# Kernel optimization log

Hardware: AMD Instinct MI355X
Metric: run time of the kernel (lower is better)

Reference implementation:

```python
import jax, jax.numpy as jnp
import numpy as np

B, T, DIN, DM, NC = 8, 4096, 1024, 256, 157
DILS = (1, 2, 4, 8, 16)


def _conv1(w, x, b=None):
    # 1x1 conv: w [out,in], x [B,in,T] -> [B,out,T]
    y = jnp.einsum('oi,bit->bot', w, x)
    return y if b is None else y + b[None, :, None]


def _dal(x, wq, wk, wv, d):
    # Dilated 3-tap multiplicative local attention (DAL block, groups=1).
    # Taps in the zero-padded (pad=d) sequence at offsets 0, d, 2d == positions t-d, t, t+d.
    _, _, T_ = x.shape
    xp = jnp.pad(x, ((0, 0), (0, 0), (d, d)))
    q = _conv1(wq, x)                 # [B,C,T]
    kp = _conv1(wk, xp)               # [B,C,T+2d]
    vp = _conv1(wv, xp)
    k = jnp.stack([kp[:, :, 0:T_], kp[:, :, d:T_ + d], kp[:, :, 2 * d:T_ + 2 * d]], axis=-1)  # [B,C,T,3]
    v = jnp.stack([vp[:, :, 0:T_], vp[:, :, d:T_ + d], vp[:, :, 2 * d:T_ + 2 * d]], axis=-1)
    attn = jax.nn.softmax(q[..., None] * k, axis=-1)  # softmax over the 3 taps
    return jnp.sum(attn * v, axis=-1)  # [B,C,T]


def _fwd(x, mask, bottle0_w, bottle0_b,
         dal1_wq, dal1_wk, dal1_wv, bottle1_w, bottle1_b,
         dal2_wq, dal2_wk, dal2_wv, bottle2_w, bottle2_b,
         dal3_wq, dal3_wk, dal3_wv, bottle3_w, bottle3_b,
         dal4_wq, dal4_wk, dal4_wv, bottle4_w, bottle4_b,
         dal5_wq, dal5_wk, dal5_wv, bottle5_w, bottle5_b,
         bottle6_w, bottle6_b):
    m = mask[:, 0:1, :]
    out = _conv1(bottle0_w, x, bottle0_b)
    layers = [
        (dal1_wq, dal1_wk, dal1_wv, bottle1_w, bottle1_b),
        (dal2_wq, dal2_wk, dal2_wv, bottle2_w, bottle2_b),
        (dal3_wq, dal3_wk, dal3_wv, bottle3_w, bottle3_b),
        (dal4_wq, dal4_wk, dal4_wv, bottle4_w, bottle4_b),
        (dal5_wq, dal5_wk, dal5_wv, bottle5_w, bottle5_b),
    ]
    # Dropout layers are identity in eval mode.
    for (wq, wk, wv, bw, bb), d in zip(layers, DILS):
        h = jax.nn.relu(_dal(out, wq, wk, wv, d))
        h = _conv1(bw, h, bb)
        out = (out + h) * m
    return _conv1(bottle6_w, out, bottle6_b) * m  # [B,NC,T]


def setup_inputs() -> dict:
    key = jax.random.key(0)
    ks = jax.random.split(key, 32)
    s = 0.05
    inp = {}
    inp['x'] = jax.random.normal(ks[0], (B, DIN, T), jnp.float32)
    inp['mask'] = jnp.ones((B, 1, T), jnp.float32)
    inp['bottle0_w'] = jax.random.normal(ks[1], (DM, DIN), jnp.float32) * s
    inp['bottle0_b'] = jnp.zeros((DM,), jnp.float32)
    i = 2
    for l in range(1, 6):
        inp['dal%d_wq' % l] = jax.random.normal(ks[i], (DM, DM), jnp.float32) * s; i += 1
        inp['dal%d_wk' % l] = jax.random.normal(ks[i], (DM, DM), jnp.float32) * s; i += 1
        inp['dal%d_wv' % l] = jax.random.normal(ks[i], (DM, DM), jnp.float32) * s; i += 1
        inp['bottle%d_w' % l] = jax.random.normal(ks[i], (DM, DM), jnp.float32) * s; i += 1
        inp['bottle%d_b' % l] = jnp.zeros((DM,), jnp.float32)
    inp['bottle6_w'] = jax.random.normal(ks[i], (NC, DM), jnp.float32) * s
    inp['bottle6_b'] = jnp.zeros((NC,), jnp.float32)
    return inp


def reference(x, mask, bottle0_w, bottle0_b,
              dal1_wq, dal1_wk, dal1_wv, bottle1_w, bottle1_b,
              dal2_wq, dal2_wk, dal2_wv, bottle2_w, bottle2_b,
              dal3_wq, dal3_wk, dal3_wv, bottle3_w, bottle3_b,
              dal4_wq, dal4_wk, dal4_wv, bottle4_w, bottle4_b,
              dal5_wq, dal5_wk, dal5_wv, bottle5_w, bottle5_b,
              bottle6_w, bottle6_b):
    return _fwd(x, mask, bottle0_w, bottle0_b,
                dal1_wq, dal1_wk, dal1_wv, bottle1_w, bottle1_b,
                dal2_wq, dal2_wk, dal2_wv, bottle2_w, bottle2_b,
                dal3_wq, dal3_wk, dal3_wv, bottle3_w, bottle3_b,
                dal4_wq, dal4_wk, dal4_wv, bottle4_w, bottle4_b,
                dal5_wq, dal5_wk, dal5_wv, bottle5_w, bottle5_b,
                bottle6_w, bottle6_b)
```

## Files before the change

### kernel.cpp

```cpp
#include <hip/hip_runtime.h>
#include <hip/hip_bf16.h>
#include <stdint.h>

#define T_LEN 4096
#define B_SZ  8
#define D_IN  1024
#define D_M   256
#define N_C   157

typedef __attribute__((ext_vector_type(8))) short short8;
typedef __attribute__((ext_vector_type(4))) float floatx4;

static __device__ __forceinline__ unsigned short f2bf(float f) {
  unsigned u = __float_as_uint(f);
  u += 0x7FFFu + ((u >> 16) & 1u);
  return (unsigned short)(u >> 16);
}
static __device__ __forceinline__ float bf2f(unsigned short h) {
  return __uint_as_float(((unsigned)h) << 16);
}

struct WSeg { const float* src; int n; int off; };
struct WPrepArgs { WSeg seg[22]; };

__global__ void wprep_kernel(WPrepArgs a, unsigned short* __restrict__ wbuf) {
  WSeg s = a.seg[blockIdx.x];
  for (int i = (blockIdx.y << 8) + threadIdx.x; i < s.n; i += (gridDim.y << 8))
    wbuf[s.off + i] = f2bf(s.src[i]);
}

__global__ void transpose_xT(const float* __restrict__ x,
                             unsigned short* __restrict__ xT) {
  __shared__ float tile[64][65];
  const int t0 = blockIdx.x << 6;
  const int i0 = blockIdx.y << 6;
  const int b  = blockIdx.z;
  const int tid = threadIdx.x;
  {
    const int row = tid >> 2;
    const int cc  = (tid & 3) << 4;
    const float* src = x + ((size_t)b * D_IN + (i0 + row)) * T_LEN + t0 + cc;
#pragma unroll
    for (int p = 0; p < 4; ++p) {
      float4 v = *(const float4*)(src + p * 4);
      tile[row][cc + p * 4 + 0] = v.x;
      tile[row][cc + p * 4 + 1] = v.y;
      tile[row][cc + p * 4 + 2] = v.z;
      tile[row][cc + p * 4 + 3] = v.w;
    }
  }
  __syncthreads();
#pragma unroll
  for (int it = 0; it < 2; ++it) {
    const int task = tid + (it << 8);
    const int tr = task >> 3;
    const int ic = (task & 7) << 3;
    short8 o;
#pragma unroll
    for (int j = 0; j < 8; ++j) o[j] = (short)f2bf(tile[ic + j][tr]);
    *(short8*)(xT + ((size_t)b * T_LEN + (t0 + tr)) * D_IN + i0 + ic) = o;
  }
}

template<bool HAS_BIAS, bool HAS_RES, bool HAS_MASK, bool WRITE_F32,
         bool WRITE_BF16, bool OUT_CT>
__global__ __launch_bounds__(256)
void gemm_kernel(const unsigned short* __restrict__ Xact,
                 const unsigned short* __restrict__ W,
                 const float* __restrict__ bias,
                 const float* __restrict__ resid,
                 const float* __restrict__ mask,
                 float* __restrict__ outF,
                 unsigned short* __restrict__ outB,
                 int K, int Mw) {
  constexpr int LDS_LD = 72;
  __shared__ unsigned short sA[128 * LDS_LD];
  __shared__ unsigned short sB[128 * LDS_LD];

  const int t0 = blockIdx.x << 7;
  const int n0 = blockIdx.y << 7;
  const int b  = blockIdx.z;
  const int tid = threadIdx.x;
  const int wv   = tid >> 6;
  const int lane = tid & 63;
  const int wm = (wv >> 1) << 6;
  const int wn = (wv & 1) << 6;
  const int fm = lane & 15;
  const int fq = lane >> 4;

  const unsigned short* Xb = Xact + (size_t)b * T_LEN * (size_t)K;

  const floatx4 fz = {0.f, 0.f, 0.f, 0.f};
  floatx4 acc[4][4];
#pragma unroll
  for (int i = 0; i < 4; ++i)
#pragma unroll
    for (int j = 0; j < 4; ++j) acc[i][j] = fz;

  for (int kk = 0; kk < K; kk += 64) {
#pragma unroll
    for (int it = 0; it < 4; ++it) {
      int c = tid + (it << 8);
      int m = c >> 3;
      int ko = (c & 7) << 3;
      *(short8*)&sA[m * LDS_LD + ko] =
          *(const short8*)(Xb + (size_t)(t0 + m) * K + (kk + ko));
    }
#pragma unroll
    for (int it = 0; it < 4; ++it) {
      int c = tid + (it << 8);
      int n = c >> 3;
      int ko = (c & 7) << 3;
      short8 val = {0, 0, 0, 0, 0, 0, 0, 0};
      if (n0 + n < Mw)
        val = *(const short8*)(W + (size_t)(n0 + n) * K + (kk + ko));
      *(short8*)&sB[n * LDS_LD + ko] = val;
    }
    __syncthreads();
#pragma unroll
    for (int ks = 0; ks < 64; ks += 32) {
      short8 af[4], bfr[4];
#pragma unroll
      for (int i = 0; i < 4; ++i)
        af[i] = *(short8*)&sA[(wm + (i << 4) + fm) * LDS_LD + ks + (fq << 3)];
#pragma unroll
      for (int j = 0; j < 4; ++j)
        bfr[j] = *(short8*)&sB[(wn + (j << 4) + fm) * LDS_LD + ks + (fq << 3)];
#pragma unroll
      for (int i = 0; i < 4; ++i)
#pragma unroll
        for (int j = 0; j < 4; ++j)
          acc[i][j] = __builtin_amdgcn_mfma_f32_16x16x32_bf16(
              af[i], bfr[j], acc[i][j], 0, 0, 0);
    }
    __syncthreads();
  }

#pragma unroll
  for (int i = 0; i < 4; ++i) {
#pragma unroll
    for (int j = 0; j < 4; ++j) {
      const int co = n0 + wn + (j << 4) + fm;
      if (co >= Mw) continue;
      const float bi = HAS_BIAS ? bias[co] : 0.0f;
#pragma unroll
      for (int r = 0; r < 4; ++r) {
        const int t = t0 + wm + (i << 4) + (fq << 2) + r;
        float val = acc[i][j][r] + bi;
        const size_t idx = ((size_t)b * T_LEN + t) * (size_t)Mw + co;
        if (HAS_RES) val += resid[idx];
        if (HAS_MASK) val *= mask[(size_t)b * T_LEN + t];
        if (WRITE_F32) {
          if (OUT_CT)
            outF[(size_t)b * Mw * T_LEN + (size_t)co * T_LEN + t] = val;
          else
            outF[idx] = val;
        }
        if (WRITE_BF16) outB[idx] = f2bf(val);
      }
    }
  }
}

__global__ void attn_kernel(const unsigned short* __restrict__ qkv,
                            unsigned short* __restrict__ hbuf, int d) {
  const int tid = threadIdx.x;
  const int t = (blockIdx.x << 3) + (tid >> 5);
  const int b = blockIdx.y;
  const int c8 = (tid & 31) << 3;
  const unsigned short* base = qkv + ((size_t)b * T_LEN + t) * 768;
  const short8 z8 = {0, 0, 0, 0, 0, 0, 0, 0};
  short8 qv = *(const short8*)(base + c8);
  short8 kc = *(const short8*)(base + 256 + c8);
  short8 vc = *(const short8*)(base + 512 + c8);
  short8 km = z8, kp = z8, vm = z8, vp = z8;
  const long off = (long)d * 768;
  if (t >= d) {
    km = *(const short8*)(base - off + 256 + c8);
    vm = *(const short8*)(base - off + 512 + c8);
  }
  if (t + d < T_LEN) {
    kp = *(const short8*)(base + off + 256 + c8);
    vp = *(const short8*)(base + off + 512 + c8);
  }
  short8 o;
#pragma unroll
  for (int e = 0; e < 8; ++e) {
    float q  = bf2f((unsigned short)qv[e]);
    float s0 = q * bf2f((unsigned short)km[e]);
    float s1 = q * bf2f((unsigned short)kc[e]);
    float s2 = q * bf2f((unsigned short)kp[e]);
    float mx = fmaxf(s0, fmaxf(s1, s2));
    float e0 = __expf(s0 - mx), e1 = __expf(s1 - mx), e2 = __expf(s2 - mx);
    float num = e0 * bf2f((unsigned short)vm[e]) +
                e1 * bf2f((unsigned short)vc[e]) +
                e2 * bf2f((unsigned short)vp[e]);
    float r = num / (e0 + e1 + e2);
    o[e] = (short)f2bf(fmaxf(r, 0.0f));
  }
  *(short8*)(hbuf + ((size_t)b * T_LEN + t) * D_M + c8) = o;
}

extern "C" void kernel_launch(void* const* d_in, const int* in_sizes, int n_in,
                              void* d_out, int out_size, void* d_ws, size_t ws_size,
                              hipStream_t stream) {
  const float* x    = (const float*)d_in[0];
  const float* mask = (const float*)d_in[1];

  char* ws = (char*)d_ws;
  unsigned short* xT   = (unsigned short*)ws;
  unsigned short* qkv  = xT;
  float*          outF = (float*)(ws + 67108864);
  unsigned short* outB = (unsigned short*)(ws + 100663296);
  unsigned short* hbuf = (unsigned short*)(ws + 117440512);
  unsigned short* wbuf = (unsigned short*)(ws + 134217728);

  const int WB0  = 0;
  const int WQKV = 262144;
  const int WBT  = 1245184;
  const int WB6  = 1572864;

  WPrepArgs pa;
  int si = 0;
  pa.seg[si++] = { (const float*)d_in[2], 262144, WB0 };
  for (int l = 0; l < 5; ++l) {
    int bi = 4 + l * 5;
    pa.seg[si++] = { (const float*)d_in[bi + 0], 65536, WQKV + l * 196608 };
    pa.seg[si++] = { (const float*)d_in[bi + 1], 65536, WQKV + l * 196608 + 65536 };
    pa.seg[si++] = { (const float*)d_in[bi + 2], 65536, WQKV + l * 196608 + 131072 };
    pa.seg[si++] = { (const float*)d_in[bi + 3], 65536, WBT + l * 65536 };
  }
  pa.seg[si++] = { (const float*)d_in[29], 40192, WB6 };

  wprep_kernel<<<dim3(22, 64), 256, 0, stream>>>(pa, wbuf);
  transpose_xT<<<dim3(64, 16, 8), 256, 0, stream>>>(x, xT);

  gemm_kernel<true, false, false, true, true, false>
      <<<dim3(32, 2, 8), 256, 0, stream>>>(
          xT, wbuf + WB0, (const float*)d_in[3], nullptr, mask,
          outF, outB, 1024, 256);

  const int dils[5] = {1, 2, 4, 8, 16};
  for (int l = 0; l < 5; ++l) {
    int bi = 4 + l * 5;
    gemm_kernel<false, false, false, false, true, false>
        <<<dim3(32, 6, 8), 256, 0, stream>>>(
            outB, wbuf + WQKV + l * 196608, nullptr, nullptr, mask,
            nullptr, qkv, 256, 768);
    attn_kernel<<<dim3(512, 8), 256, 0, stream>>>(qkv, hbuf, dils[l]);
    gemm_kernel<true, true, true, true, true, false>
        <<<dim3(32, 2, 8), 256, 0, stream>>>(
            hbuf, wbuf + WBT + l * 65536, (const float*)d_in[bi + 4], outF, mask,
            outF, outB, 256, 256);
  }

  gemm_kernel<true, false, true, true, false, true>
      <<<dim3(32, 2, 8), 256, 0, stream>>>(
          outB, wbuf + WB6, (const float*)d_in[30], nullptr, mask,
          (float*)d_out, nullptr, 256, 157);
}
```

Baseline: 726.0 us.

## Fuse attention into bottleneck GEMM A-load and keep residual in bf16

The separate attention kernel is removed, and the dilated 3-tap softmax is now computed while staging the A operand of the following 1x1-conv GEMM. This drops the hbuf round trip and one launch per layer. The fp32 residual stream is also dropped: the residual is read from the bf16 buffer and written back in place. The grid is reordered so output-channel blocks of the same time tile run next to each other, which should help L2 reuse. As a cost, the attention math is repeated for every output-channel block (two for the 256-wide GEMM), and the residual now accumulates in bf16, which loses precision.

Measured after the change: 723.2 us. Within noise of the previous version (-0.4%).

```diff
diff --git a/kernel.cpp b/kernel.cpp
--- a/kernel.cpp
+++ b/kernel.cpp
@@ -62,23 +62,23 @@
   }
 }
 
-template<bool HAS_BIAS, bool HAS_RES, bool HAS_MASK, bool WRITE_F32,
-         bool WRITE_BF16, bool OUT_CT>
+template<bool ATTN, bool HAS_BIAS, bool HAS_RES, bool HAS_MASK,
+         bool WRITE_BF16, bool OUT_CT_F32>
 __global__ __launch_bounds__(256)
 void gemm_kernel(const unsigned short* __restrict__ Xact,
                  const unsigned short* __restrict__ W,
                  const float* __restrict__ bias,
-                 const float* __restrict__ resid,
+                 const unsigned short* __restrict__ residB,
                  const float* __restrict__ mask,
                  float* __restrict__ outF,
                  unsigned short* __restrict__ outB,
-                 int K, int Mw) {
+                 int K, int Mw, int dil) {
   constexpr int LDS_LD = 72;
   __shared__ unsigned short sA[128 * LDS_LD];
   __shared__ unsigned short sB[128 * LDS_LD];
 
-  const int t0 = blockIdx.x << 7;
-  const int n0 = blockIdx.y << 7;
+  const int n0 = blockIdx.x << 7;
+  const int t0 = blockIdx.y << 7;
   const int b  = blockIdx.z;
   const int tid = threadIdx.x;
   const int wv   = tid >> 6;
@@ -88,8 +88,10 @@
   const int fm = lane & 15;
   const int fq = lane >> 4;
 
-  const unsigned short* Xb = Xact + (size_t)b * T_LEN * (size_t)K;
-
+  const unsigned short* Xb =
+      Xact + (size_t)b * T_LEN * (size_t)(ATTN ? 768 : K);
+
+  const short8 z8 = {0, 0, 0, 0, 0, 0, 0, 0};
   const floatx4 fz = {0.f, 0.f, 0.f, 0.f};
   floatx4 acc[4][4];
 #pragma unroll
@@ -98,20 +100,60 @@
     for (int j = 0; j < 4; ++j) acc[i][j] = fz;
 
   for (int kk = 0; kk < K; kk += 64) {
-#pragma unroll
-    for (int it = 0; it < 4; ++it) {
-      int c = tid + (it << 8);
-      int m = c >> 3;
-      int ko = (c & 7) << 3;
-      *(short8*)&sA[m * LDS_LD + ko] =
-          *(const short8*)(Xb + (size_t)(t0 + m) * K + (kk + ko));
+    if constexpr (ATTN) {
+#pragma unroll
+      for (int it = 0; it < 4; ++it) {
+        int c = tid + (it << 8);
+        int m = c >> 3;
+        int ch = kk + ((c & 7) << 3);
+        int t = t0 + m;
+        const unsigned short* base = Xb + (size_t)t * 768 + ch;
+        short8 qv = *(const short8*)(base);
+        short8 kc = *(const short8*)(base + 256);
+        short8 vc = *(const short8*)(base + 512);
+        short8 km = z8, kp = z8, vm = z8, vp = z8;
+        const long off = (long)dil * 768;
+        if (t >= dil) {
+          km = *(const short8*)(base - off + 256);
+          vm = *(const short8*)(base - off + 512);
+        }
+        if (t + dil < T_LEN) {
+          kp = *(const short8*)(base + off + 256);
+          vp = *(const short8*)(base + off + 512);
+        }
+        short8 o;
+#pragma unroll
+        for (int e = 0; e < 8; ++e) {
+          float q  = bf2f((unsigned short)qv[e]);
+          float s0 = q * bf2f((unsigned short)km[e]);
+          float s1 = q * bf2f((unsigned short)kc[e]);
+          float s2 = q * bf2f((unsigned short)kp[e]);
+          float mx = fmaxf(s0, fmaxf(s1, s2));
+          float e0 = __expf(s0 - mx), e1 = __expf(s1 - mx), e2 = __expf(s2 - mx);
+          float num = e0 * bf2f((unsigned short)vm[e]) +
+                      e1 * bf2f((unsigned short)vc[e]) +
+                      e2 * bf2f((unsigned short)vp[e]);
+          float r = num / (e0 + e1 + e2);
+          o[e] = (short)f2bf(fmaxf(r, 0.0f));
+        }
+        *(short8*)&sA[m * LDS_LD + (ch - kk)] = o;
+      }
+    } else {
+#pragma unroll
+      for (int it = 0; it < 4; ++it) {
+        int c = tid + (it << 8);
+        int m = c >> 3;
+        int ko = (c & 7) << 3;
+        *(short8*)&sA[m * LDS_LD + ko] =
+            *(const short8*)(Xb + (size_t)(t0 + m) * K + (kk + ko));
+      }
     }
 #pragma unroll
     for (int it = 0; it < 4; ++it) {
       int c = tid + (it << 8);
       int n = c >> 3;
       int ko = (c & 7) << 3;
-      short8 val = {0, 0, 0, 0, 0, 0, 0, 0};
+      short8 val = z8;
       if (n0 + n < Mw)
         val = *(const short8*)(W + (size_t)(n0 + n) * K + (kk + ko));
       *(short8*)&sB[n * LDS_LD + ko] = val;
@@ -148,57 +190,14 @@
         const int t = t0 + wm + (i << 4) + (fq << 2) + r;
         float val = acc[i][j][r] + bi;
         const size_t idx = ((size_t)b * T_LEN + t) * (size_t)Mw + co;
-        if (HAS_RES) val += resid[idx];
+        if (HAS_RES) val += bf2f(residB[idx]);
         if (HAS_MASK) val *= mask[(size_t)b * T_LEN + t];
-        if (WRITE_F32) {
-          if (OUT_CT)
-            outF[(size_t)b * Mw * T_LEN + (size_t)co * T_LEN + t] = val;
-          else
-            outF[idx] = val;
-        }
+        if (OUT_CT_F32)
+          outF[(size_t)b * Mw * T_LEN + (size_t)co * T_LEN + t] = val;
         if (WRITE_BF16) outB[idx] = f2bf(val);
       }
     }
   }
-}
-
-__global__ void attn_kernel(const unsigned short* __restrict__ qkv,
-                            unsigned short* __restrict__ hbuf, int d) {
-  const int tid = threadIdx.x;
-  const int t = (blockIdx.x << 3) + (tid >> 5);
-  const int b = blockIdx.y;
-  const int c8 = (tid & 31) << 3;
-  const unsigned short* base = qkv + ((size_t)b * T_LEN + t) * 768;
-  const short8 z8 = {0, 0, 0, 0, 0, 0, 0, 0};
-  short8 qv = *(const short8*)(base + c8);
-  short8 kc = *(const short8*)(base + 256 + c8);
-  short8 vc = *(const short8*)(base + 512 + c8);
-  short8 km = z8, kp = z8, vm = z8, vp = z8;
-  const long off = (long)d * 768;
-  if (t >= d) {
-    km = *(const short8*)(base - off + 256 + c8);
-    vm = *(const short8*)(base - off + 512 + c8);
-  }
-  if (t + d < T_LEN) {
-    kp = *(const short8*)(base + off + 256 + c8);
-    vp = *(const short8*)(base + off + 512 + c8);
-  }
-  short8 o;
-#pragma unroll
-  for (int e = 0; e < 8; ++e) {
-    float q  = bf2f((unsigned short)qv[e]);
-    float s0 = q * bf2f((unsigned short)km[e]);
-    float s1 = q * bf2f((unsigned short)kc[e]);
-    float s2 = q * bf2f((unsigned short)kp[e]);
-    float mx = fmaxf(s0, fmaxf(s1, s2));
-    float e0 = __expf(s0 - mx), e1 = __expf(s1 - mx), e2 = __expf(s2 - mx);
-    float num = e0 * bf2f((unsigned short)vm[e]) +
-                e1 * bf2f((unsigned short)vc[e]) +
-                e2 * bf2f((unsigned short)vp[e]);
-    float r = num / (e0 + e1 + e2);
-    o[e] = (short)f2bf(fmaxf(r, 0.0f));
-  }
-  *(short8*)(hbuf + ((size_t)b * T_LEN + t) * D_M + c8) = o;
 }
 
 extern "C" void kernel_launch(void* const* d_in, const int* in_sizes, int n_in,
@@ -210,10 +209,8 @@
   char* ws = (char*)d_ws;
   unsigned short* xT   = (unsigned short*)ws;
   unsigned short* qkv  = xT;
-  float*          outF = (float*)(ws + 67108864);
-  unsigned short* outB = (unsigned short*)(ws + 100663296);
-  unsigned short* hbuf = (unsigned short*)(ws + 117440512);
-  unsigned short* wbuf = (unsigned short*)(ws + 134217728);
+  unsigned short* outB = (unsigned short*)(ws + 67108864);
+  unsigned short* wbuf = (unsigned short*)(ws + 83886080);
 
   const int WB0  = 0;
   const int WQKV = 262144;
@@ -235,27 +232,26 @@
   wprep_kernel<<<dim3(22, 64), 256, 0, stream>>>(pa, wbuf);
   transpose_xT<<<dim3(64, 16, 8), 256, 0, stream>>>(x, xT);
 
-  gemm_kernel<true, false, false, true, true, false>
-      <<<dim3(32, 2, 8), 256, 0, stream>>>(
+  gemm_kernel<false, true, false, false, true, false>
+      <<<dim3(2, 32, 8), 256, 0, stream>>>(
           xT, wbuf + WB0, (const float*)d_in[3], nullptr, mask,
-          outF, outB, 1024, 256);
+          nullptr, outB, 1024, 256, 0);
 
   const int dils[5] = {1, 2, 4, 8, 16};
   for (int l = 0; l < 5; ++l) {
     int bi = 4 + l * 5;
     gemm_kernel<false, false, false, false, true, false>
-        <<<dim3(32, 6, 8), 256, 0, stream>>>(
+        <<<dim3(6, 32, 8), 256, 0, stream>>>(
             outB, wbuf + WQKV + l * 196608, nullptr, nullptr, mask,
-            nullptr, qkv, 256, 768);
-    attn_kernel<<<dim3(512, 8), 256, 0, stream>>>(qkv, hbuf, dils[l]);
+            nullptr, qkv, 256, 768, 0);
     gemm_kernel<true, true, true, true, true, false>
-        <<<dim3(32, 2, 8), 256, 0, stream>>>(
-            hbuf, wbuf + WBT + l * 65536, (const float*)d_in[bi + 4], outF, mask,
-            outF, outB, 256, 256);
-  }
-
-  gemm_kernel<true, false, true, true, false, true>
-      <<<dim3(32, 2, 8), 256, 0, stream>>>(
+        <<<dim3(2, 32, 8), 256, 0, stream>>>(
+            qkv, wbuf + WBT + l * 65536, (const float*)d_in[bi + 4], outB, mask,
+            nullptr, outB, 256, 256, dils[l]);
+  }
+
+  gemm_kernel<false, true, false, true, false, true>
+      <<<dim3(2, 32, 8), 256, 0, stream>>>(
           outB, wbuf + WB6, (const float*)d_in[30], nullptr, mask,
-          (float*)d_out, nullptr, 256, 157);
-}
+          (float*)d_out, nullptr, 256, 157, 0);
+}
```
